# Optimization experiments

Hardware: AMD Instinct MI355X
Metric: run time of the kernel (lower is better)

## Reference

```python
import jax, jax.numpy as jnp
import numpy as np

INPUT_DIM = 4096
OUTPUT_DIM = 4096
N_MAG_BITS = 3  # inference_sequence = [0, 3]: magnitude bits 0..2, sign bit at index 3
N_TOKENS = 8192
DESIRED_STD = np.sqrt(2.0 / INPUT_DIM)  # kaiming fan_in std target


def _ste(hard, soft):
    # straight-through estimator: forward = hard, backward = identity on soft
    return soft + jax.lax.stop_gradient(hard - soft)


def to_bit(x):
    # latent float -> {0,1} bit plane
    return _ste((x >= 0).astype(x.dtype), x)


def to_sign(x):
    # latent float -> {-1,+1} sign plane
    return _ste(jnp.where(x >= 0, 1.0, -1.0).astype(x.dtype), x)


def setup_inputs() -> dict:
    key = jax.random.key(0)
    k1, k2, k3 = jax.random.split(key, 3)
    x = jax.random.normal(k1, (N_TOKENS, INPUT_DIM), dtype=jnp.float32)
    mag = jax.random.normal(k2, (N_MAG_BITS, INPUT_DIM, OUTPUT_DIM), dtype=jnp.float32)
    sign_bit = jax.random.normal(k3, (INPUT_DIM, OUTPUT_DIM), dtype=jnp.float32)
    return {"x": x, "mag": mag, "sign_bit": sign_bit}


def reference(x, mag, sign_bit):
    # calculate_number: reconstruct weight from bit planes
    # w = sign * sum_i bit_i * 2^{-(i+1)}
    bits = to_bit(mag)  # [K, in, out]
    place = (2.0 ** -(jnp.arange(1, N_MAG_BITS + 1, dtype=jnp.float32)))  # [K]
    magnitude = jnp.einsum("kio,k->io", bits, place)
    w = to_sign(sign_bit) * magnitude  # [in, out]
    # calc_scaling_factor on detached weight (cpu/numpy round-trip in original -> constant)
    alpha = DESIRED_STD / (jnp.std(jax.lax.stop_gradient(w)) + 1e-12)
    w = w * alpha
    # F.linear(x, W.T) == x @ W
    return jnp.matmul(x, w)
```

## Files before the change

kernel.cpp:

```cpp
#include <hip/hip_runtime.h>
#include <hip/hip_bf16.h>
#include <cstdint>
#include <cstddef>

#define IN_DIM 4096
#define OUT_DIM 4096
#define NTOK 8192
#define PLANE (IN_DIM * OUT_DIM)
#define NPACK_BLOCKS 4096

typedef int i32x4_t __attribute__((ext_vector_type(4)));

__device__ inline void async_load16(void* lds, const void* g) {
    __builtin_amdgcn_global_load_lds(
        (const __attribute__((address_space(1))) char*)g,
        (__attribute__((address_space(3))) char*)lds,
        16, 0, 0);
}

__global__ __launch_bounds__(256) void pack_kernel(const float* __restrict__ mag,
                                                   const float* __restrict__ sgn,
                                                   signed char* __restrict__ wT,
                                                   int* __restrict__ partials) {
    __shared__ short tile[64 * 68];
    __shared__ int red2[4], reds[4];
    const int t = threadIdx.x;
    const int o0 = blockIdx.x * 64, i0 = blockIdx.y * 64;
    const int oq = t & 15, ir = t >> 4;
    int lk2 = 0, lsk = 0;
    #pragma unroll
    for (int r = 0; r < 4; ++r) {
        const int ilo = r * 16 + ir;
        const size_t idx = (size_t)(i0 + ilo) * OUT_DIM + o0 + oq * 4;
        const float4 m0 = *(const float4*)(mag + idx);
        const float4 m1 = *(const float4*)(mag + idx + (size_t)PLANE);
        const float4 m2 = *(const float4*)(mag + idx + 2 * (size_t)PLANE);
        const float4 sv = *(const float4*)(sgn + idx);
        short4 c;
        {
            int k = ((m0.x >= 0.f) ? 4 : 0) | ((m1.x >= 0.f) ? 2 : 0) | ((m2.x >= 0.f) ? 1 : 0);
            int cd = (sv.x >= 0.f) ? k : -k; lk2 += k * k; lsk += cd; c.x = (short)cd;
        }
        {
            int k = ((m0.y >= 0.f) ? 4 : 0) | ((m1.y >= 0.f) ? 2 : 0) | ((m2.y >= 0.f) ? 1 : 0);
            int cd = (sv.y >= 0.f) ? k : -k; lk2 += k * k; lsk += cd; c.y = (short)cd;
        }
        {
            int k = ((m0.z >= 0.f) ? 4 : 0) | ((m1.z >= 0.f) ? 2 : 0) | ((m2.z >= 0.f) ? 1 : 0);
            int cd = (sv.z >= 0.f) ? k : -k; lk2 += k * k; lsk += cd; c.z = (short)cd;
        }
        {
            int k = ((m0.w >= 0.f) ? 4 : 0) | ((m1.w >= 0.f) ? 2 : 0) | ((m2.w >= 0.f) ? 1 : 0);
            int cd = (sv.w >= 0.f) ? k : -k; lk2 += k * k; lsk += cd; c.w = (short)cd;
        }
        *(short4*)&tile[ilo * 68 + oq * 4] = c;
    }
    #pragma unroll
    for (int off = 32; off > 0; off >>= 1) {
        lk2 += __shfl_down(lk2, off);
        lsk += __shfl_down(lsk, off);
    }
    const int wv = t >> 6, ln = t & 63;
    if (ln == 0) { red2[wv] = lk2; reds[wv] = lsk; }
    __syncthreads();
    if (t == 0) {
        const int bid = blockIdx.y * gridDim.x + blockIdx.x;
        partials[bid] = red2[0] + red2[1] + red2[2] + red2[3];
        partials[NPACK_BLOCKS + bid] = reds[0] + reds[1] + reds[2] + reds[3];
    }
    const int iq = t & 15, orr = t >> 4;
    #pragma unroll
    for (int r = 0; r < 4; ++r) {
        const int olo = r * 16 + orr;
        char4 w4;
        w4.x = (signed char)tile[(iq * 4 + 0) * 68 + olo];
        w4.y = (signed char)tile[(iq * 4 + 1) * 68 + olo];
        w4.z = (signed char)tile[(iq * 4 + 2) * 68 + olo];
        w4.w = (signed char)tile[(iq * 4 + 3) * 68 + olo];
        *(char4*)&wT[(size_t)(o0 + olo) * IN_DIM + i0 + iq * 4] = w4;
    }
}

__global__ __launch_bounds__(256) void alpha_kernel(const int* __restrict__ partials,
                                                    float* __restrict__ alpha8) {
    __shared__ int red2[4], reds[4];
    const int t = threadIdx.x;
    int k2 = 0, sk = 0;
    for (int i = t; i < NPACK_BLOCKS; i += 256) {
        k2 += partials[i];
        sk += partials[NPACK_BLOCKS + i];
    }
    #pragma unroll
    for (int off = 32; off > 0; off >>= 1) {
        k2 += __shfl_down(k2, off);
        sk += __shfl_down(sk, off);
    }
    const int wv = t >> 6, ln = t & 63;
    if (ln == 0) { red2[wv] = k2; reds[wv] = sk; }
    __syncthreads();
    if (t == 0) {
        const double n = (double)PLANE;
        const double sumk2 = (double)(red2[0] + red2[1] + red2[2] + red2[3]);
        const double sumsk = (double)(reds[0] + reds[1] + reds[2] + reds[3]);
        const double mean = sumsk / (8.0 * n);
        const double e2 = sumk2 / (64.0 * n);
        const double sd = sqrt(e2 - mean * mean);
        *alpha8 = (float)(sqrt(2.0 / (double)IN_DIM) / (sd + 1e-12) * 0.125);
    }
}

__global__ __launch_bounds__(256) void quant_kernel(const float* __restrict__ x,
                                                    signed char* __restrict__ xq,
                                                    float* __restrict__ steps) {
    __shared__ float red[4];
    const int r = blockIdx.x, t = threadIdx.x;
    const float* xr = x + (size_t)r * IN_DIM;
    float4 v[4];
    float am = 0.f;
    #pragma unroll
    for (int p = 0; p < 4; ++p) {
        v[p] = ((const float4*)xr)[p * 256 + t];
        am = fmaxf(am, fmaxf(fmaxf(fabsf(v[p].x), fabsf(v[p].y)),
                             fmaxf(fabsf(v[p].z), fabsf(v[p].w))));
    }
    #pragma unroll
    for (int off = 32; off > 0; off >>= 1) am = fmaxf(am, __shfl_down(am, off));
    const int wv = t >> 6, ln = t & 63;
    if (ln == 0) red[wv] = am;
    __syncthreads();
    am = fmaxf(fmaxf(red[0], red[1]), fmaxf(red[2], red[3]));
    am = fmaxf(am, 1e-30f);
    const float rstep = 127.0f / am;
    if (t == 0) steps[r] = am * (1.0f / 127.0f);
    int* xqi = (int*)(xq + (size_t)r * IN_DIM);
    #pragma unroll
    for (int p = 0; p < 4; ++p) {
        const int q0 = (int)rintf(v[p].x * rstep);
        const int q1 = (int)rintf(v[p].y * rstep);
        const int q2 = (int)rintf(v[p].z * rstep);
        const int q3 = (int)rintf(v[p].w * rstep);
        xqi[p * 256 + t] = (q0 & 0xFF) | ((q1 & 0xFF) << 8) | ((q2 & 0xFF) << 16) | (q3 << 24);
    }
}

__global__ __launch_bounds__(256) void gemm_kernel(const signed char* __restrict__ A,
                                                   const signed char* __restrict__ B,
                                                   float* __restrict__ C,
                                                   const float* __restrict__ alphap,
                                                   const float* __restrict__ steps) {
    __shared__ __align__(16) signed char As[128 * 64];
    __shared__ __align__(16) signed char Bs[128 * 64];
    const int t = threadIdx.x;
    const int lane = t & 63, wave = t >> 6;
    const int wm = wave >> 1, wn = wave & 1;
    const int m0 = blockIdx.y * 128, n0 = blockIdx.x * 128;
    const int r15 = lane & 15, q = lane >> 4;

    i32x4_t acc[4][4] = {};

    int aoff[4], boff[4];
    #pragma unroll
    for (int i = 0; i < 4; ++i) {
        aoff[i] = (wm * 64 + i * 16 + r15) * 64 + q * 16;
        boff[i] = (wn * 64 + i * 16 + r15) * 64 + q * 16;
    }

    const int c0 = t, c1 = t + 256;
    const int row0 = c0 >> 2, cb0 = (c0 & 3) * 16;
    const int row1 = c1 >> 2, cb1 = (c1 & 3) * 16;

    for (int k0 = 0; k0 < IN_DIM; k0 += 64) {
        async_load16(&As[c0 * 16], A + (size_t)(m0 + row0) * IN_DIM + k0 + cb0);
        async_load16(&As[c1 * 16], A + (size_t)(m0 + row1) * IN_DIM + k0 + cb1);
        async_load16(&Bs[c0 * 16], B + (size_t)(n0 + row0) * IN_DIM + k0 + cb0);
        async_load16(&Bs[c1 * 16], B + (size_t)(n0 + row1) * IN_DIM + k0 + cb1);
        __syncthreads();
        i32x4_t a[4], b[4];
        #pragma unroll
        for (int i = 0; i < 4; ++i) a[i] = *(const i32x4_t*)&As[aoff[i]];
        #pragma unroll
        for (int i = 0; i < 4; ++i) b[i] = *(const i32x4_t*)&Bs[boff[i]];
        #pragma unroll
        for (int mt = 0; mt < 4; ++mt)
            #pragma unroll
            for (int nt = 0; nt < 4; ++nt)
                acc[mt][nt] = __builtin_amdgcn_mfma_i32_16x16x64_i8(a[mt], b[nt], acc[mt][nt], 0, 0, 0);
        __syncthreads();
    }

    const float alpha8 = *alphap;
    #pragma unroll
    for (int mt = 0; mt < 4; ++mt) {
        const int mbase = m0 + wm * 64 + mt * 16 + q * 4;
        const float s0 = alpha8 * steps[mbase + 0];
        const float s1 = alpha8 * steps[mbase + 1];
        const float s2 = alpha8 * steps[mbase + 2];
        const float s3 = alpha8 * steps[mbase + 3];
        #pragma unroll
        for (int nt = 0; nt < 4; ++nt) {
            const int n = n0 + wn * 64 + nt * 16 + r15;
            float* cp = C + (size_t)mbase * OUT_DIM + n;
            cp[0 * OUT_DIM] = (float)acc[mt][nt][0] * s0;
            cp[1 * OUT_DIM] = (float)acc[mt][nt][1] * s1;
            cp[2 * OUT_DIM] = (float)acc[mt][nt][2] * s2;
            cp[3 * OUT_DIM] = (float)acc[mt][nt][3] * s3;
        }
    }
}

extern "C" void kernel_launch(void* const* d_in, const int* in_sizes, int n_in,
                              void* d_out, int out_size, void* d_ws, size_t ws_size,
                              hipStream_t stream) {
    const float* x   = (const float*)d_in[0];
    const float* mag = (const float*)d_in[1];
    const float* sgn = (const float*)d_in[2];
    float* out = (float*)d_out;

    char* ws = (char*)d_ws;
    int* partials = (int*)ws;
    float* alphap = (float*)(ws + 32768);
    float* steps  = (float*)(ws + 65536);
    signed char* wT = (signed char*)(ws + 131072);
    signed char* xq = (signed char*)(ws + 131072 + (size_t)PLANE);

    pack_kernel<<<dim3(OUT_DIM / 64, IN_DIM / 64), 256, 0, stream>>>(mag, sgn, wT, partials);
    quant_kernel<<<NTOK, 256, 0, stream>>>(x, xq, steps);
    alpha_kernel<<<1, 256, 0, stream>>>(partials, alphap);
    gemm_kernel<<<dim3(OUT_DIM / 128, NTOK / 128), 256, 0, stream>>>(xq, wT, out, alphap, steps);
}
```

Before: 580.1 us.

## Restructure int8 GEMM with 256x256 tiles, 4-stage async pipeline, swizzled LDS

```diff
diff --git a/kernel.cpp b/kernel.cpp
--- a/kernel.cpp
+++ b/kernel.cpp
@@ -8,6 +8,11 @@
 #define NTOK 8192
 #define PLANE (IN_DIM * OUT_DIM)
 #define NPACK_BLOCKS 4096
+
+#define BM 256
+#define BN 256
+#define BK 64
+#define KTILES (IN_DIM / BK)
 
 typedef int i32x4_t __attribute__((ext_vector_type(4)));
 
@@ -143,55 +148,100 @@
     }
 }
 
-__global__ __launch_bounds__(256) void gemm_kernel(const signed char* __restrict__ A,
-                                                   const signed char* __restrict__ B,
-                                                   float* __restrict__ C,
-                                                   const float* __restrict__ alphap,
-                                                   const float* __restrict__ steps) {
-    __shared__ __align__(16) signed char As[128 * 64];
-    __shared__ __align__(16) signed char Bs[128 * 64];
+__global__ __launch_bounds__(512, 2) void gemm_kernel(const signed char* __restrict__ A,
+                                                      const signed char* __restrict__ B,
+                                                      float* __restrict__ C,
+                                                      const float* __restrict__ alphap,
+                                                      const float* __restrict__ steps) {
+    __shared__ __align__(16) signed char As[4][BM * BK];
+    __shared__ __align__(16) signed char Bs[4][BN * BK];
     const int t = threadIdx.x;
-    const int lane = t & 63, wave = t >> 6;
-    const int wm = wave >> 1, wn = wave & 1;
-    const int m0 = blockIdx.y * 128, n0 = blockIdx.x * 128;
+    const int lane = t & 63;
+    const int wave = t >> 6;
+    const int wm = wave >> 2, wn = wave & 3;
     const int r15 = lane & 15, q = lane >> 4;
 
-    i32x4_t acc[4][4] = {};
-
-    int aoff[4], boff[4];
+    const int raw = blockIdx.x;
+    const int wg = (raw & 7) * 64 + (raw >> 3);
+    const int m0 = (wg >> 4) * BM;
+    const int n0 = (wg & 15) * BN;
+
+    int aoff[8], boff[4];
+    #pragma unroll
+    for (int i = 0; i < 8; ++i) {
+        const int r = wm * 128 + i * 16 + r15;
+        aoff[i] = r * BK + ((q ^ ((r >> 1) & 3)) << 4);
+    }
     #pragma unroll
     for (int i = 0; i < 4; ++i) {
-        aoff[i] = (wm * 64 + i * 16 + r15) * 64 + q * 16;
-        boff[i] = (wn * 64 + i * 16 + r15) * 64 + q * 16;
-    }
-
-    const int c0 = t, c1 = t + 256;
-    const int row0 = c0 >> 2, cb0 = (c0 & 3) * 16;
-    const int row1 = c1 >> 2, cb1 = (c1 & 3) * 16;
-
-    for (int k0 = 0; k0 < IN_DIM; k0 += 64) {
-        async_load16(&As[c0 * 16], A + (size_t)(m0 + row0) * IN_DIM + k0 + cb0);
-        async_load16(&As[c1 * 16], A + (size_t)(m0 + row1) * IN_DIM + k0 + cb1);
-        async_load16(&Bs[c0 * 16], B + (size_t)(n0 + row0) * IN_DIM + k0 + cb0);
-        async_load16(&Bs[c1 * 16], B + (size_t)(n0 + row1) * IN_DIM + k0 + cb1);
-        __syncthreads();
-        i32x4_t a[4], b[4];
-        #pragma unroll
-        for (int i = 0; i < 4; ++i) a[i] = *(const i32x4_t*)&As[aoff[i]];
-        #pragma unroll
-        for (int i = 0; i < 4; ++i) b[i] = *(const i32x4_t*)&Bs[boff[i]];
-        #pragma unroll
-        for (int mt = 0; mt < 4; ++mt)
-            #pragma unroll
-            for (int nt = 0; nt < 4; ++nt)
-                acc[mt][nt] = __builtin_amdgcn_mfma_i32_16x16x64_i8(a[mt], b[nt], acc[mt][nt], 0, 0, 0);
-        __syncthreads();
-    }
+        const int r = wn * 64 + i * 16 + r15;
+        boff[i] = r * BK + ((q ^ ((r >> 1) & 3)) << 4);
+    }
+
+    const int c0 = t, c1 = t + 512;
+    const int ra0 = c0 >> 2, ra1 = c1 >> 2;
+    const int sc0 = (((c0 & 3) ^ ((c0 >> 3) & 3)) << 4);
+    const int sc1 = (((c1 & 3) ^ ((c1 >> 3) & 3)) << 4);
+    const size_t srcA0 = (size_t)(m0 + ra0) * IN_DIM + sc0;
+    const size_t srcA1 = (size_t)(m0 + ra1) * IN_DIM + sc1;
+    const size_t srcB0 = (size_t)(n0 + ra0) * IN_DIM + sc0;
+    const size_t srcB1 = (size_t)(n0 + ra1) * IN_DIM + sc1;
+
+    i32x4_t acc[8][4] = {};
+
+#define STAGE(kt, buf) do {                                          \
+        const int koff_ = (kt) * BK;                                 \
+        async_load16(&As[buf][c0 * 16], A + srcA0 + koff_);          \
+        async_load16(&As[buf][c1 * 16], A + srcA1 + koff_);          \
+        async_load16(&Bs[buf][c0 * 16], B + srcB0 + koff_);          \
+        async_load16(&Bs[buf][c1 * 16], B + srcB1 + koff_);          \
+    } while (0)
+
+#define COMPUTE(buf) do {                                            \
+        i32x4_t a_[8], b_[4];                                        \
+        _Pragma("unroll")                                            \
+        for (int i = 0; i < 8; ++i)                                  \
+            a_[i] = *(const i32x4_t*)&As[buf][aoff[i]];              \
+        _Pragma("unroll")                                            \
+        for (int i = 0; i < 4; ++i)                                  \
+            b_[i] = *(const i32x4_t*)&Bs[buf][boff[i]];              \
+        __builtin_amdgcn_s_setprio(1);                               \
+        _Pragma("unroll")                                            \
+        for (int mt = 0; mt < 8; ++mt)                               \
+            _Pragma("unroll")                                        \
+            for (int nt = 0; nt < 4; ++nt)                           \
+                acc[mt][nt] = __builtin_amdgcn_mfma_i32_16x16x64_i8( \
+                    a_[mt], b_[nt], acc[mt][nt], 0, 0, 0);           \
+        __builtin_amdgcn_s_setprio(0);                               \
+    } while (0)
+
+    STAGE(0, 0); STAGE(1, 1); STAGE(2, 2);
+
+    #pragma unroll 4
+    for (int kt = 0; kt < KTILES - 3; ++kt) {
+        STAGE(kt + 3, (kt + 3) & 3);
+        asm volatile("s_waitcnt vmcnt(12)" ::: "memory");
+        __builtin_amdgcn_s_barrier();
+        COMPUTE(kt & 3);
+        __builtin_amdgcn_s_barrier();
+    }
+    asm volatile("s_waitcnt vmcnt(8)" ::: "memory");
+    __builtin_amdgcn_s_barrier();
+    COMPUTE((KTILES - 3) & 3);
+    asm volatile("s_waitcnt vmcnt(4)" ::: "memory");
+    __builtin_amdgcn_s_barrier();
+    COMPUTE((KTILES - 2) & 3);
+    asm volatile("s_waitcnt vmcnt(0)" ::: "memory");
+    __builtin_amdgcn_s_barrier();
+    COMPUTE((KTILES - 1) & 3);
+
+#undef STAGE
+#undef COMPUTE
 
     const float alpha8 = *alphap;
     #pragma unroll
-    for (int mt = 0; mt < 4; ++mt) {
-        const int mbase = m0 + wm * 64 + mt * 16 + q * 4;
+    for (int mt = 0; mt < 8; ++mt) {
+        const int mbase = m0 + wm * 128 + mt * 16 + q * 4;
         const float s0 = alpha8 * steps[mbase + 0];
         const float s1 = alpha8 * steps[mbase + 1];
         const float s2 = alpha8 * steps[mbase + 2];
@@ -226,5 +276,5 @@
     pack_kernel<<<dim3(OUT_DIM / 64, IN_DIM / 64), 256, 0, stream>>>(mag, sgn, wT, partials);
     quant_kernel<<<NTOK, 256, 0, stream>>>(x, xq, steps);
     alpha_kernel<<<1, 256, 0, stream>>>(partials, alphap);
-    gemm_kernel<<<dim3(OUT_DIM / 128, NTOK / 128), 256, 0, stream>>>(xq, wT, out, alphap, steps);
-}
+    gemm_kernel<<<dim3((NTOK / BM) * (OUT_DIM / BN)), 512, 0, stream>>>(xq, wT, out, alphap, steps);
+}
```

New measurement: 553.1 us. 1.05x faster.
